# Performance work log

Hardware: AMD Instinct MI355X
Metric: run time of the kernel (lower is better)

The kernel has to match this reference:

```python
import jax, jax.numpy as jnp
import numpy as np
import math

B, C, N, T = 8, 128, 256, 64  # batch, d_model, nodes, timesteps
H = 8                          # attention heads
NUM_STEPS = 50                 # diffusion steps


def _conv2d(x, w, b):
    # Conv2d with kernel (1,3), padding (0,1); x: (B,C,N,T), w: (O,I,1,3)
    y = jax.lax.conv_general_dilated(x, w, (1, 1), [(0, 0), (1, 1)],
                                     dimension_numbers=('NCHW', 'OIHW', 'NCHW'))
    return y + b[None, :, None, None]


def _linear(x, w, b=None):
    y = jnp.einsum('...i,oi->...o', x, w)
    return y if b is None else y + b


def _ln(x, g, b, eps=1e-5):
    m = jnp.mean(x, -1, keepdims=True)
    v = jnp.var(x, -1, keepdims=True)
    return (x - m) * jax.lax.rsqrt(v + eps) * g + b


def _forward(step, x, adj, wq, bq, wk, bk, w1, b1, w2, b2, theta,
             ln0_g, ln0_b, ln1_g, ln1_b, p1_w, p1_b, p2_w, p2_b,
             dxc_w, dxc_b, dec_w, dec_b, dc1_w, dc1_b, dp2_w, dp2_b):
    dk = C // H
    sq = 1.0 / math.sqrt(dk)
    sc = 1.0 / math.sqrt(C)
    # ---- normalized graph Laplacian: D^{-1/2} A D^{-1/2} (get_laplacian, normalize=True)
    d = jnp.sum(adj, -1) ** -0.5
    Lap = adj * d[:, None] * d[None, :]  # (N,N)
    # ---- temporal attention with conv-derived Q/K (MultiHeadAttentionAwareTemporal)
    q = _conv2d(x, wq, bq).reshape(B, H, dk, N, T).transpose(0, 3, 1, 4, 2)  # (B,N,H,T,dk)
    k = _conv2d(x, wk, bk).reshape(B, H, dk, N, T).transpose(0, 3, 1, 4, 2)
    v = _linear(x.transpose(0, 2, 3, 1), w1, b1).reshape(B, N, T, H, dk).transpose(0, 1, 3, 2, 4)
    p = jax.nn.softmax(jnp.einsum('bnhtd,bnhsd->bnhts', q, k) * sq, axis=-1)
    o = jnp.einsum('bnhts,bnhsd->bnhtd', p, v).transpose(0, 1, 3, 2, 4).reshape(B, N, T, C)
    xp = x.transpose(0, 2, 3, 1) + _ln(_linear(o, w2, b2), ln0_g, ln0_b)  # (B,N,T,C)
    # ---- spatial attention GCN (Spatial_Attention_layer + spatialAttentionGCN)
    xt = xp.transpose(0, 2, 1, 3)  # (B,T,N,C)
    sat = jax.nn.softmax(jnp.einsum('btnf,btmf->btnm', xt, xt) * sc, axis=-1) * sc
    y = jnp.einsum('btnm,btmf->btnf', Lap[None, None] * sat, xt)
    y = jax.nn.relu(_linear(y, theta)).transpose(0, 2, 1, 3)  # (B,N,T,C)
    h = xp + _ln(y, ln1_g, ln1_b)
    # ---- diffusion step embedding (DiffusionEmbedding)
    dim = C // 2
    freqs = 10.0 ** (jnp.arange(dim, dtype=jnp.float32) / (dim - 1) * 4.0)
    tab = jnp.arange(NUM_STEPS, dtype=jnp.float32)[:, None] * freqs[None, :]
    tab = jnp.concatenate([jnp.sin(tab), jnp.cos(tab)], -1)  # (NUM_STEPS, C)
    e = jax.nn.silu(_linear(tab[step], p1_w, p1_b))
    e = jax.nn.silu(_linear(e, p2_w, p2_b))  # (B,C)
    h = h + e[:, None, None, :]
    # ---- Decoder: conv + sigmoid-gated add + relu + 1x1 projection to 2 channels
    enc = h.transpose(0, 3, 1, 2)  # (B,C,N,T)
    xh = _conv2d(enc, dxc_w, dxc_b)
    ec = _conv2d(enc, dec_w, dec_b)
    out = jax.nn.relu(xh + jax.nn.sigmoid(ec) + _conv2d(ec, dc1_w, dc1_b))
    out = jnp.einsum('bcnt,oc->bont', out, dp2_w) + dp2_b[None, :, None, None]  # (B,2,N,T)
    return out


def setup_inputs() -> dict:
    key = jax.random.key(0)
    ks = iter(jax.random.split(key, 40))
    s = 1.0 / math.sqrt(C)
    sk = 1.0 / math.sqrt(3 * C)

    def nrm(shape, scale):
        return jax.random.normal(next(ks), shape, jnp.float32) * scale

    return {
        'x': nrm((B, C, N, T), 1.0),
        'adj': jax.random.uniform(next(ks), (N, N), jnp.float32, 0.1, 1.0),
        'step': jax.random.randint(next(ks), (B,), 0, NUM_STEPS, jnp.int32),
        'wq': nrm((C, C, 1, 3), sk), 'bq': jnp.zeros((C,), jnp.float32),
        'wk': nrm((C, C, 1, 3), sk), 'bk': jnp.zeros((C,), jnp.float32),
        'w1': nrm((C, C), s), 'b1': jnp.zeros((C,), jnp.float32),
        'w2': nrm((C, C), s), 'b2': jnp.zeros((C,), jnp.float32),
        'theta': nrm((C, C), s),
        'ln0_g': jnp.ones((C,), jnp.float32), 'ln0_b': jnp.zeros((C,), jnp.float32),
        'ln1_g': jnp.ones((C,), jnp.float32), 'ln1_b': jnp.zeros((C,), jnp.float32),
        'p1_w': nrm((C, C), s), 'p1_b': jnp.zeros((C,), jnp.float32),
        'p2_w': nrm((C, C), s), 'p2_b': jnp.zeros((C,), jnp.float32),
        'dxc_w': nrm((C, C, 1, 3), sk), 'dxc_b': jnp.zeros((C,), jnp.float32),
        'dec_w': nrm((C, C, 1, 3), sk), 'dec_b': jnp.zeros((C,), jnp.float32),
        'dc1_w': nrm((C, C, 1, 3), sk), 'dc1_b': jnp.zeros((C,), jnp.float32),
        'dp2_w': nrm((2, C), s), 'dp2_b': jnp.zeros((2,), jnp.float32),
    }


def reference(x, adj, step, wq, bq, wk, bk, w1, b1, w2, b2, theta,
              ln0_g, ln0_b, ln1_g, ln1_b, p1_w, p1_b, p2_w, p2_b,
              dxc_w, dxc_b, dec_w, dec_b, dc1_w, dc1_b, dp2_w, dp2_b):
    return _forward(step, x, adj, wq, bq, wk, bk, w1, b1, w2, b2, theta,
                    ln0_g, ln0_b, ln1_g, ln1_b, p1_w, p1_b, p2_w, p2_b,
                    dxc_w, dxc_b, dec_w, dec_b, dc1_w, dc1_b, dp2_w, dp2_b)
```

## Files before the change

### kernel.cpp

```cpp
#include <hip/hip_runtime.h>
#include <hip/hip_bf16.h>

namespace {

constexpr int C = 128, N = 256, T = 64, Bsz = 8;
constexpr int TILE = T * C;
constexpr size_t BIGE = (size_t)Bsz * N * T * C;

typedef short v8s __attribute__((ext_vector_type(8)));
typedef float v4f __attribute__((ext_vector_type(4)));

__device__ __forceinline__ float bfu(unsigned short u) {
  unsigned int x = ((unsigned int)u) << 16;
  return __uint_as_float(x);
}
__device__ __forceinline__ unsigned short f2b(float v) {
  __hip_bfloat16 h = __float2bfloat16(v);
  return *(unsigned short*)&h;
}
__device__ __forceinline__ unsigned int pk2(float a, float b) {
  return (unsigned int)f2b(a) | ((unsigned int)f2b(b) << 16);
}
__device__ __forceinline__ float ld(const void* p, size_t i, int f32) {
  if (f32) return ((const float*)p)[i];
  return bfu(((const unsigned short*)p)[i]);
}
__device__ __forceinline__ float sigm(float x) { return 1.f / (1.f + __expf(-x)); }

__global__ __launch_bounds__(64) void k_sniff(const unsigned short* x, int* flag) {
  __shared__ int cnt[64];
  int tid = threadIdx.x;
  int c = 0;
  for (int u = 0; u < 8; ++u) {
    unsigned short v = x[tid * 8 + u];
    int e = (v >> 7) & 255;
    c += (e >= 97 && e <= 157) ? 1 : 0;
  }
  cnt[tid] = c;
  __syncthreads();
  if (tid == 0) {
    int s = 0;
    for (int i = 0; i < 64; ++i) s += cnt[i];
    flag[0] = (s < 435) ? 1 : 0;
  }
}

struct PrepArgs {
  const int* flag;
  const void *wq, *wk, *w1, *w2, *th, *dxc, *dec, *dc1;
  const void *bq, *bk, *b1, *b2, *l0g, *l0b, *l1g, *l1b, *dxcb, *decb, *dc1b, *dp2w, *dp2b;
  unsigned short *wqkB, *w1B, *w2B;
  __hip_bfloat16* thB;
  unsigned short *decWb, *dxcWb, *dc1Wb;
  float *bqk, *b1f, *b2f, *l0gf, *l0bf, *l1gf, *l1bf, *dxcbf, *decbf, *dc1bf, *dp2wf, *dp2bf;
};

__global__ __launch_bounds__(256) void k_prepall(
    PrepArgs a, const void* adj, float* lap, const int* step,
    const void* p1w, const void* p1b, const void* p2w, const void* p2b, float* e) {
  __shared__ float sh[256];
  __shared__ float e1[128];
  int f = a.flag[0];
  int blk = blockIdx.x, tid = threadIdx.x;
  if (blk < 128) {
    int idx = blk * 256 + tid;
    const int stride = 32768;
    for (int i = idx; i < 256 * 384; i += stride) {
      int o = i / 384, k = i - o * 384;
      int j = k >> 7, ii = k & 127;
      float v = (o < 128) ? ld(a.wq, (o * 128 + ii) * 3 + j, f)
                          : ld(a.wk, ((o - 128) * 128 + ii) * 3 + j, f);
      a.wqkB[i] = f2b(v);
    }
    for (int i = idx; i < 16384; i += stride) {
      a.w1B[i] = f2b(ld(a.w1, i, f));
      a.w2B[i] = f2b(ld(a.w2, i, f));
      a.thB[i] = __float2bfloat16(ld(a.th, i, f));
    }
    for (int i = idx; i < 16384; i += stride) {
      int o = i >> 7, ii = i & 127;
      int sbase = (o * 128 + ii) * 3;
#pragma unroll
      for (int j = 0; j < 3; ++j) {
        int dsti = o * 384 + j * 128 + ii;
        a.decWb[dsti] = f2b(ld(a.dec, sbase + j, f));
        a.dxcWb[dsti] = f2b(ld(a.dxc, sbase + j, f));
        a.dc1Wb[dsti] = f2b(ld(a.dc1, sbase + j, f));
      }
    }
    for (int i = idx; i < 256; i += stride) {
      a.bqk[i] = (i < 128) ? ld(a.bq, i, f) : ld(a.bk, i - 128, f);
      a.dp2wf[i] = ld(a.dp2w, i, f);
    }
    for (int i = idx; i < 128; i += stride) {
      a.b1f[i] = ld(a.b1, i, f);   a.b2f[i] = ld(a.b2, i, f);
      a.l0gf[i] = ld(a.l0g, i, f); a.l0bf[i] = ld(a.l0b, i, f);
      a.l1gf[i] = ld(a.l1g, i, f); a.l1bf[i] = ld(a.l1b, i, f);
      a.dxcbf[i] = ld(a.dxcb, i, f); a.decbf[i] = ld(a.decb, i, f); a.dc1bf[i] = ld(a.dc1b, i, f);
    }
    if (idx < 2) a.dp2bf[idx] = ld(a.dp2b, idx, f);
  } else if (blk < 192) {
    float s = 0.f;
    for (int m = 0; m < 256; ++m) s += ld(adj, tid * 256 + m, f);
    sh[tid] = 1.f / sqrtf(s);
    __syncthreads();
    int n0 = (blk - 128) * 4;
    for (int idx = tid; idx < 1024; idx += 256) {
      int n = n0 + (idx >> 8), m = idx & 255;
      lap[n * 256 + m] = ld(adj, n * 256 + m, f) * sh[n] * sh[m];
    }
  } else {
    int b = blk - 192;
    if (tid < 128) {
      float sv = (float)step[b];
      int i0 = tid & 63;
      float fr = powf(10.f, (float)i0 / 63.f * 4.f);
      float ang = sv * fr;
      sh[tid] = (tid < 64) ? sinf(ang) : cosf(ang);
    }
    __syncthreads();
    if (tid < 128) {
      float aa = ld(p1b, tid, f);
      for (int i = 0; i < 128; ++i) aa += sh[i] * ld(p1w, tid * 128 + i, f);
      aa = aa * sigm(aa);
      e1[tid] = aa;
    }
    __syncthreads();
    if (tid < 128) {
      float a2 = ld(p2b, tid, f);
      for (int i = 0; i < 128; ++i) a2 += e1[i] * ld(p2w, tid * 128 + i, f);
      e[b * 128 + tid] = a2 * sigm(a2);
    }
  }
}

constexpr int XBS = 136;
constexpr int VTS = 72;

__global__ __launch_bounds__(512, 4) void k_mega1(
    const void* xin, const int* flag,
    const unsigned short* wqkB, const float* bqk,
    const unsigned short* w1B, const float* b1f,
    const unsigned short* w2B, const float* b2f,
    const float* l0g, const float* l0b, float* g0) {
  int bn = blockIdx.x, b = bn >> 8, n = bn & 255;
  __shared__ unsigned short Xb[66 * XBS];
  __shared__ unsigned short qo[64 * XBS];
  __shared__ unsigned short kls[64 * XBS];
  __shared__ unsigned short vT[128 * VTS];
  __shared__ float pS[8 * 64], pQ[8 * 64];
  __shared__ float mrow[64], vrow[64];
  int tid = threadIdx.x;
  int wv = tid >> 6, lane = tid & 63, quad = lane >> 4, lr = lane & 15;
  int f = flag[0];
  int hb = wv * 16;
  const v8s zz = {0, 0, 0, 0, 0, 0, 0, 0};
  {
    size_t xoff = (size_t)b * C * N * T + (size_t)n * T;
    for (int idx = tid * 4; idx < TILE; idx += 2048) {
      int i = idx >> 6, t = idx & 63;
      unsigned short pk[4];
      if (f) {
        float4 v4 = *(const float4*)&((const float*)xin)[xoff + (size_t)i * N * T + t];
        pk[0] = f2b(v4.x); pk[1] = f2b(v4.y); pk[2] = f2b(v4.z); pk[3] = f2b(v4.w);
      } else {
        ushort4 u4 = *(const ushort4*)&((const unsigned short*)xin)[xoff + (size_t)i * N * T + t];
        pk[0] = u4.x; pk[1] = u4.y; pk[2] = u4.z; pk[3] = u4.w;
      }
#pragma unroll
      for (int u = 0; u < 4; ++u) Xb[(t + u + 1) * XBS + i] = pk[u];
    }
    if (tid < 128) { Xb[tid] = 0; Xb[65 * XBS + tid] = 0; }
  }
  __syncthreads();
  {
    int mt0 = wv * 2;
    v4f acc[2][4];
#pragma unroll
    for (int mi = 0; mi < 2; ++mi)
#pragma unroll
      for (int nt = 0; nt < 4; ++nt) acc[mi][nt] = (v4f){0.f, 0.f, 0.f, 0.f};
    for (int j = 0; j < 3; ++j) {
#pragma unroll
      for (int kt = 0; kt < 4; ++kt) {
        int ko = j * 128 + kt * 32 + quad * 8;
        v8s a0 = *(const v8s*)&wqkB[(mt0 * 16 + lr) * 384 + ko];
        v8s a1 = *(const v8s*)&wqkB[((mt0 + 1) * 16 + lr) * 384 + ko];
        int bko = kt * 32 + quad * 8;
#pragma unroll
        for (int nt = 0; nt < 4; ++nt) {
          v8s bb = *(const v8s*)&Xb[(nt * 16 + lr + j) * XBS + bko];
          acc[0][nt] = __builtin_amdgcn_mfma_f32_16x16x32_bf16(a0, bb, acc[0][nt], 0, 0, 0);
          acc[1][nt] = __builtin_amdgcn_mfma_f32_16x16x32_bf16(a1, bb, acc[1][nt], 0, 0, 0);
        }
      }
    }
    unsigned short* dst = (wv < 4) ? qo : kls;
#pragma unroll
    for (int mi = 0; mi < 2; ++mi) {
      int og = (mt0 + mi) * 16 + quad * 4;
      int oo = og & 127;
#pragma unroll
      for (int nt = 0; nt < 4; ++nt) {
        int t = nt * 16 + lr;
        *(unsigned int*)&dst[t * XBS + oo] =
            pk2(acc[mi][nt][0] + bqk[og], acc[mi][nt][1] + bqk[og + 1]);
        *(unsigned int*)&dst[t * XBS + oo + 2] =
            pk2(acc[mi][nt][2] + bqk[og + 2], acc[mi][nt][3] + bqk[og + 3]);
      }
    }
  }
  {
    v4f av[4];
#pragma unroll
    for (int nt = 0; nt < 4; ++nt) av[nt] = (v4f){0.f, 0.f, 0.f, 0.f};
#pragma unroll
    for (int kt = 0; kt < 4; ++kt) {
      int ko = kt * 32 + quad * 8;
      v8s a = *(const v8s*)&w1B[(wv * 16 + lr) * 128 + ko];
#pragma unroll
      for (int nt = 0; nt < 4; ++nt) {
        v8s bb = *(const v8s*)&Xb[(nt * 16 + lr + 1) * XBS + ko];
        av[nt] = __builtin_amdgcn_mfma_f32_16x16x32_bf16(a, bb, av[nt], 0, 0, 0);
      }
    }
#pragma unroll
    for (int nt = 0; nt < 4; ++nt) {
      int t = nt * 16 + lr;
#pragma unroll
      for (int r = 0; r < 4; ++r) {
        int o = hb + quad * 4 + r;
        vT[o * VTS + t] = f2b(av[nt][r] + b1f[o]);
      }
    }
  }
  __syncthreads();
  {
    v4f sa[4][4];
#pragma unroll
    for (int ms = 0; ms < 4; ++ms)
#pragma unroll
      for (int nt = 0; nt < 4; ++nt) sa[ms][nt] = (v4f){0.f, 0.f, 0.f, 0.f};
    {
      v8s afs[4], bfs[4];
#pragma unroll
      for (int ms = 0; ms < 4; ++ms)
        afs[ms] = (quad < 2) ? *(const v8s*)&kls[(ms * 16 + lr) * XBS + hb + quad * 8] : zz;
#pragma unroll
      for (int nt = 0; nt < 4; ++nt)
        bfs[nt] = (quad < 2) ? *(const v8s*)&qo[(nt * 16 + lr) * XBS + hb + quad * 8] : zz;
#pragma unroll
      for (int ms = 0; ms < 4; ++ms)
#pragma unroll
        for (int nt = 0; nt < 4; ++nt)
          sa[ms][nt] = __builtin_amdgcn_mfma_f32_16x16x32_bf16(afs[ms], bfs[nt], sa[ms][nt], 0, 0, 0);
    }
#pragma unroll
    for (int nt = 0; nt < 4; ++nt) {
      float mx = -1e30f;
#pragma unroll
      for (int ms = 0; ms < 4; ++ms)
#pragma unroll
        for (int r = 0; r < 4; ++r) {
          float v = sa[ms][nt][r] * 0.25f;
          sa[ms][nt][r] = v;
          mx = fmaxf(mx, v);
        }
      mx = fmaxf(mx, __shfl_xor(mx, 16, 64));
      mx = fmaxf(mx, __shfl_xor(mx, 32, 64));
      float ssum = 0.f;
#pragma unroll
      for (int ms = 0; ms < 4; ++ms)
#pragma unroll
        for (int r = 0; r < 4; ++r) {
          float e = __expf(sa[ms][nt][r] - mx);
          sa[ms][nt][r] = e;
          ssum += e;
        }
      ssum += __shfl_xor(ssum, 16, 64);
      ssum += __shfl_xor(ssum, 32, 64);
      float inv = 1.f / ssum;
#pragma unroll
      for (int ms = 0; ms < 4; ++ms)
#pragma unroll
        for (int r = 0; r < 4; ++r) sa[ms][nt][r] *= inv;
    }
    v4f ov[4];
#pragma unroll
    for (int nt = 0; nt < 4; ++nt) ov[nt] = (v4f){0.f, 0.f, 0.f, 0.f};
#pragma unroll
    for (int kt = 0; kt < 2; ++kt) {
      unsigned int pA[4][2], pB[4][2];
#pragma unroll
      for (int nt = 0; nt < 4; ++nt) {
#pragma unroll
        for (int h = 0; h < 2; ++h) {
          pA[nt][h] = pk2(sa[2 * kt][nt][2 * h], sa[2 * kt][nt][2 * h + 1]);
          pB[nt][h] = pk2(sa[2 * kt + 1][nt][2 * h], sa[2 * kt + 1][nt][2 * h + 1]);
        }
      }
      v8s aV = *(const v8s*)&vT[(hb + lr) * VTS + kt * 32 + quad * 8];
#pragma unroll
      for (int nt = 0; nt < 4; ++nt) {
        union { unsigned int u[4]; v8s s; } bu;
#pragma unroll
        for (int w = 0; w < 4; ++w) {
          int src = (2 * (quad & 1) + (w >> 1)) * 16 + lr;
          unsigned int x0 = (unsigned int)__shfl((int)pA[nt][w & 1], src, 64);
          unsigned int x1 = (unsigned int)__shfl((int)pB[nt][w & 1], src, 64);
          bu.u[w] = (quad >> 1) ? x1 : x0;
        }
        ov[nt] = __builtin_amdgcn_mfma_f32_16x16x32_bf16(aV, bu.s, ov[nt], 0, 0, 0);
      }
    }
#pragma unroll
    for (int nt = 0; nt < 4; ++nt) {
      int t = nt * 16 + lr;
      *(unsigned int*)&qo[t * XBS + hb + quad * 4] = pk2(ov[nt][0], ov[nt][1]);
      *(unsigned int*)&qo[t * XBS + hb + quad * 4 + 2] = pk2(ov[nt][2], ov[nt][3]);
    }
  }
  __syncthreads();
  v4f aw[4];
  {
#pragma unroll
    for (int nt = 0; nt < 4; ++nt) aw[nt] = (v4f){0.f, 0.f, 0.f, 0.f};
#pragma unroll
    for (int kt = 0; kt < 4; ++kt) {
      int ko = kt * 32 + quad * 8;
      v8s a = *(const v8s*)&w2B[(wv * 16 + lr) * 128 + ko];
#pragma unroll
      for (int nt = 0; nt < 4; ++nt) {
        v8s bb = *(const v8s*)&qo[(nt * 16 + lr) * XBS + ko];
        aw[nt] = __builtin_amdgcn_mfma_f32_16x16x32_bf16(a, bb, aw[nt], 0, 0, 0);
      }
    }
    int ob = hb + quad * 4;
#pragma unroll
    for (int nt = 0; nt < 4; ++nt) {
      float s = 0.f, q2 = 0.f;
#pragma unroll
      for (int r = 0; r < 4; ++r) {
        aw[nt][r] += b2f[ob + r];
        s += aw[nt][r];
        q2 += aw[nt][r] * aw[nt][r];
      }
      s += __shfl_xor(s, 16, 64);  s += __shfl_xor(s, 32, 64);
      q2 += __shfl_xor(q2, 16, 64); q2 += __shfl_xor(q2, 32, 64);
      if (quad == 0) {
        pS[wv * 64 + nt * 16 + lr] = s;
        pQ[wv * 64 + nt * 16 + lr] = q2;
      }
    }
  }
  __syncthreads();
  if (tid < 64) {
    float s = 0.f, q2 = 0.f;
#pragma unroll
    for (int w = 0; w < 8; ++w) { s += pS[w * 64 + tid]; q2 += pQ[w * 64 + tid]; }
    float mm = s * (1.f / 128.f);
    mrow[tid] = mm;
    vrow[tid] = rsqrtf(q2 * (1.f / 128.f) - mm * mm + 1e-5f);
  }
  __syncthreads();
  {
    int ob = hb + quad * 4;
    float gg[4], bb2[4];
#pragma unroll
    for (int r = 0; r < 4; ++r) { gg[r] = l0g[ob + r]; bb2[r] = l0b[ob + r]; }
    float* dst = g0 + (size_t)bn * TILE;
#pragma unroll
    for (int nt = 0; nt < 4; ++nt) {
      int t = nt * 16 + lr;
      float m = mrow[t], rs = vrow[t];
      ushort4 xr = *(const ushort4*)&Xb[(t + 1) * XBS + ob];
      float4 o4;
      o4.x = (aw[nt][0] - m) * rs * gg[0] + bb2[0] + bfu(xr.x);
      o4.y = (aw[nt][1] - m) * rs * gg[1] + bb2[1] + bfu(xr.y);
      o4.z = (aw[nt][2] - m) * rs * gg[2] + bb2[2] + bfu(xr.z);
      o4.w = (aw[nt][3] - m) * rs * gg[3] + bb2[3] + bfu(xr.w);
      *(float4*)&dst[t * 128 + ob] = o4;
    }
  }
}

constexpr int XS = 136;
constexpr int TS = 264;

__global__ __launch_bounds__(512, 1) void k_megasp(
    const float* g0, const float* lap, const unsigned short* thB,
    const float* l1g, const float* l1b, const float* e, unsigned short* g0b) {
  int bt = blockIdx.x, b = bt >> 6, t = bt & 63;
  __shared__ unsigned short R1[256 * XS];
  __shared__ unsigned short R2[256 * XS];
  __shared__ float pS[8][256], pQ[8][256];
  __shared__ float mrow[256], vrow[256];
  unsigned short* Xhi = R1;
  unsigned short* Xlo = R2;
  unsigned short* Xt = R2;
  unsigned short* Pld = R1;
  int tid = threadIdx.x;
  int wv = tid >> 6, lane = tid & 63, quad = lane >> 4, lr = lane & 15;
  int wrow0 = wv * 32;
  const float sc = 0.08838834764831845f;
  {
    size_t base = (size_t)b * (N * (size_t)TILE) + (size_t)t * 128;
    for (int idx = tid * 4; idx < 32768; idx += 2048) {
      int n = idx >> 7, c = idx & 127;
      float4 v4 = *(const float4*)&g0[base + (size_t)n * TILE + c];
      ushort4 h, l;
      h.x = f2b(v4.x); l.x = f2b(v4.x - bfu(h.x));
      h.y = f2b(v4.y); l.y = f2b(v4.y - bfu(h.y));
      h.z = f2b(v4.z); l.z = f2b(v4.z - bfu(h.z));
      h.w = f2b(v4.w); l.w = f2b(v4.w - bfu(h.w));
      *(ushort4*)&Xhi[n * XS + c] = h;
      *(ushort4*)&Xlo[n * XS + c] = l;
    }
  }
  __syncthreads();
  v4f acc[2][16];
#pragma unroll
  for (int mi = 0; mi < 2; ++mi)
#pragma unroll
    for (int nt = 0; nt < 16; ++nt) acc[mi][nt] = (v4f){0.f, 0.f, 0.f, 0.f};
  for (int kt = 0; kt < 4; ++kt) {
    int ko = kt * 32 + quad * 8;
    v8s ah0 = *(const v8s*)&Xhi[(wrow0 + lr) * XS + ko];
    v8s al0 = *(const v8s*)&Xlo[(wrow0 + lr) * XS + ko];
    v8s ah1 = *(const v8s*)&Xhi[(wrow0 + 16 + lr) * XS + ko];
    v8s al1 = *(const v8s*)&Xlo[(wrow0 + 16 + lr) * XS + ko];
#pragma unroll
    for (int nt = 0; nt < 16; ++nt) {
      v8s bh = *(const v8s*)&Xhi[(nt * 16 + lr) * XS + ko];
      v8s bl = *(const v8s*)&Xlo[(nt * 16 + lr) * XS + ko];
      acc[0][nt] = __builtin_amdgcn_mfma_f32_16x16x32_bf16(ah0, bh, acc[0][nt], 0, 0, 0);
      acc[0][nt] = __builtin_amdgcn_mfma_f32_16x16x32_bf16(ah0, bl, acc[0][nt], 0, 0, 0);
      acc[0][nt] = __builtin_amdgcn_mfma_f32_16x16x32_bf16(al0, bh, acc[0][nt], 0, 0, 0);
      acc[1][nt] = __builtin_amdgcn_mfma_f32_16x16x32_bf16(ah1, bh, acc[1][nt], 0, 0, 0);
      acc[1][nt] = __builtin_amdgcn_mfma_f32_16x16x32_bf16(ah1, bl, acc[1][nt], 0, 0, 0);
      acc[1][nt] = __builtin_amdgcn_mfma_f32_16x16x32_bf16(al1, bh, acc[1][nt], 0, 0, 0);
    }
  }
  __syncthreads();
  for (int task = tid; task < 8192; task += 512) {
    int c = task & 127, n0 = (task >> 7) * 4;
    ushort4 w;
    w.x = Xhi[(n0 + 0) * XS + c];
    w.y = Xhi[(n0 + 1) * XS + c];
    w.z = Xhi[(n0 + 2) * XS + c];
    w.w = Xhi[(n0 + 3) * XS + c];
    *(ushort4*)&Xt[c * TS + n0] = w;
  }
  __syncthreads();
  unsigned int pk1[2][8][2];
#pragma unroll
  for (int mi = 0; mi < 2; ++mi) {
#pragma unroll
    for (int r = 0; r < 4; ++r) {
      int row = wrow0 + 16 * mi + quad * 4 + r;
      float mx = -1e30f;
#pragma unroll
      for (int nt = 0; nt < 16; ++nt) {
        acc[mi][nt][r] *= sc;
        mx = fmaxf(mx, acc[mi][nt][r]);
      }
#pragma unroll
      for (int m = 8; m > 0; m >>= 1) mx = fmaxf(mx, __shfl_xor(mx, m, 16));
      float ex[16];
      float ssum = 0.f;
#pragma unroll
      for (int nt = 0; nt < 16; ++nt) { ex[nt] = __expf(acc[mi][nt][r] - mx); ssum += ex[nt]; }
#pragma unroll
      for (int m = 8; m > 0; m >>= 1) ssum += __shfl_xor(ssum, m, 16);
      float inv = sc / ssum;
      const float* lrow = lap + row * 256 + lr;
#pragma unroll
      for (int nt = 0; nt < 8; ++nt)
        Pld[row * XS + nt * 16 + lr] = f2b(ex[nt] * inv * lrow[nt * 16]);
#pragma unroll
      for (int nt = 8; nt < 16; ++nt) {
        unsigned int hbw = (unsigned int)f2b(ex[nt] * inv * lrow[nt * 16]);
        if ((r & 1) == 0) pk1[mi][nt - 8][r >> 1] = hbw;
        else pk1[mi][nt - 8][r >> 1] |= hbw << 16;
      }
    }
  }
  v4f acc2[2][8];
#pragma unroll
  for (int mi = 0; mi < 2; ++mi)
#pragma unroll
    for (int nt = 0; nt < 8; ++nt) acc2[mi][nt] = (v4f){0.f, 0.f, 0.f, 0.f};
#pragma unroll
  for (int h = 0; h < 2; ++h) {
    if (h == 1) {
#pragma unroll
      for (int mi = 0; mi < 2; ++mi) {
        int rowb = wrow0 + 16 * mi + quad * 4;
#pragma unroll
        for (int k = 0; k < 8; ++k) {
          int col = k * 16 + lr;
          unsigned int u0 = pk1[mi][k][0], u1 = pk1[mi][k][1];
          Pld[(rowb + 0) * XS + col] = (unsigned short)u0;
          Pld[(rowb + 1) * XS + col] = (unsigned short)(u0 >> 16);
          Pld[(rowb + 2) * XS + col] = (unsigned short)u1;
          Pld[(rowb + 3) * XS + col] = (unsigned short)(u1 >> 16);
        }
      }
    }
    for (int kt = 0; kt < 4; ++kt) {
      int ko = kt * 32 + quad * 8;
      v8s pa0 = *(const v8s*)&Pld[(wrow0 + lr) * XS + ko];
      v8s pa1 = *(const v8s*)&Pld[(wrow0 + 16 + lr) * XS + ko];
#pragma unroll
      for (int nt = 0; nt < 8; ++nt) {
        v8s xb = *(const v8s*)&Xt[(nt * 16 + lr) * TS + h * 128 + ko];
        acc2[0][nt] = __builtin_amdgcn_mfma_f32_16x16x32_bf16(pa0, xb, acc2[0][nt], 0, 0, 0);
        acc2[1][nt] = __builtin_amdgcn_mfma_f32_16x16x32_bf16(pa1, xb, acc2[1][nt], 0, 0, 0);
      }
    }
  }
  __syncthreads();
  unsigned short* yB = R2;
  unsigned short* ths = R1;
#pragma unroll
  for (int mi = 0; mi < 2; ++mi) {
    int nb = wrow0 + 16 * mi + quad * 4;
#pragma unroll
    for (int nt = 0; nt < 8; ++nt) {
      int c = nt * 16 + lr;
#pragma unroll
      for (int r = 0; r < 4; ++r)
        yB[(nb + r) * XS + c] = f2b(acc2[mi][nt][r]);
    }
  }
  for (int idx = tid * 8; idx < 16384; idx += 4096) {
    int o = idx >> 7, k = idx & 127;
    *(uint4*)&ths[o * 136 + k] = *(const uint4*)&thB[idx];
  }
  __syncthreads();
  v4f acc3[16];
#pragma unroll
  for (int nt = 0; nt < 16; ++nt) acc3[nt] = (v4f){0.f, 0.f, 0.f, 0.f};
#pragma unroll
  for (int kt = 0; kt < 4; ++kt) {
    int ko = kt * 32 + quad * 8;
    v8s a = *(const v8s*)&ths[(wv * 16 + lr) * 136 + ko];
#pragma unroll
    for (int nt = 0; nt < 16; ++nt) {
      v8s bb = *(const v8s*)&yB[(nt * 16 + lr) * XS + ko];
      acc3[nt] = __builtin_amdgcn_mfma_f32_16x16x32_bf16(a, bb, acc3[nt], 0, 0, 0);
    }
  }
#pragma unroll
  for (int nt = 0; nt < 16; ++nt) {
    float s = 0.f, q2 = 0.f;
#pragma unroll
    for (int r = 0; r < 4; ++r) {
      float v = fmaxf(acc3[nt][r], 0.f);
      acc3[nt][r] = v;
      s += v; q2 += v * v;
    }
    s += __shfl_xor(s, 16, 64);  s += __shfl_xor(s, 32, 64);
    q2 += __shfl_xor(q2, 16, 64); q2 += __shfl_xor(q2, 32, 64);
    if (quad == 0) { pS[wv][nt * 16 + lr] = s; pQ[wv][nt * 16 + lr] = q2; }
  }
  __syncthreads();
  if (tid < 256) {
    float s = 0.f, q2 = 0.f;
#pragma unroll
    for (int w = 0; w < 8; ++w) { s += pS[w][tid]; q2 += pQ[w][tid]; }
    float mm = s * (1.f / 128.f);
    mrow[tid] = mm;
    vrow[tid] = rsqrtf(q2 * (1.f / 128.f) - mm * mm + 1e-5f);
  }
  __syncthreads();
  {
    int o0 = wv * 16 + quad * 4;
    float gg[4], bb2[4], ev[4];
    const float* eb = e + b * 128;
#pragma unroll
    for (int r = 0; r < 4; ++r) { gg[r] = l1g[o0 + r]; bb2[r] = l1b[o0 + r]; ev[r] = eb[o0 + r]; }
#pragma unroll
    for (int nt = 0; nt < 16; ++nt) {
      int n = nt * 16 + lr;
      float m = mrow[n], rs = vrow[n];
      size_t ga = ((size_t)(b * 256 + n)) * TILE + (size_t)t * 128 + o0;
      float4 xa = *(const float4*)&g0[ga];
      ushort4 pk;
      pk.x = f2b((acc3[nt][0] - m) * rs * gg[0] + bb2[0] + xa.x + ev[0]);
      pk.y = f2b((acc3[nt][1] - m) * rs * gg[1] + bb2[1] + xa.y + ev[1]);
      pk.z = f2b((acc3[nt][2] - m) * rs * gg[2] + bb2[2] + xa.z + ev[2]);
      pk.w = f2b((acc3[nt][3] - m) * rs * gg[3] + bb2[3] + xa.w + ev[3]);
      *(ushort4*)&g0b[ga] = pk;
    }
  }
}

__global__ __launch_bounds__(512, 4) void k_megadec(
    const unsigned short* g0b, const unsigned short* decW, const float* decb,
    const unsigned short* dxcW, const float* dxcb,
    const unsigned short* dc1W, const float* dc1b,
    const float* dp2w, const float* dp2b, const int* flag, void* outv) {
  int bn = blockIdx.x, b = bn >> 8, n = bn & 255;
  int f32o = flag[0];
  __shared__ unsigned short Xm[66 * XBS];
  __shared__ unsigned short E2[66 * XBS];
  __shared__ float pb0[8][64], pb1[8][64];
  int tid = threadIdx.x;
  int wv = tid >> 6, lane = tid & 63, quad = lane >> 4, lr = lane & 15;
  int m0 = wv * 16;
  const unsigned short* gp = g0b + (size_t)bn * TILE;
  for (int idx = tid * 8; idx < TILE; idx += 4096) {
    int t = idx >> 7, c = idx & 127;
    *(uint4*)&Xm[(t + 1) * XBS + c] = *(const uint4*)&gp[idx];
  }
  if (tid < 128) {
    Xm[tid] = 0; Xm[65 * XBS + tid] = 0;
    E2[tid] = 0; E2[65 * XBS + tid] = 0;
  }
  __syncthreads();
  v4f acc[4];
  float ecv[4][4];
#pragma unroll
  for (int nt = 0; nt < 4; ++nt) acc[nt] = (v4f){0.f, 0.f, 0.f, 0.f};
  for (int j = 0; j < 3; ++j) {
#pragma unroll
    for (int kt = 0; kt < 4; ++kt) {
      v8s a = *(const v8s*)&decW[(m0 + lr) * 384 + j * 128 + kt * 32 + quad * 8];
      int bko = kt * 32 + quad * 8;
#pragma unroll
      for (int nt = 0; nt < 4; ++nt) {
        v8s bb = *(const v8s*)&Xm[(nt * 16 + lr + j) * XBS + bko];
        acc[nt] = __builtin_amdgcn_mfma_f32_16x16x32_bf16(a, bb, acc[nt], 0, 0, 0);
      }
    }
  }
#pragma unroll
  for (int nt = 0; nt < 4; ++nt) {
    int t = nt * 16 + lr;
    int o = m0 + quad * 4;
    ushort4 pk;
#pragma unroll
    for (int r = 0; r < 4; ++r) {
      float v = acc[nt][r] + decb[o + r];
      ecv[nt][r] = v;
      ((unsigned short*)&pk)[r] = f2b(v);
    }
    *(ushort4*)&E2[(t + 1) * XBS + o] = pk;
  }
  __syncthreads();
  v4f ax[4], ac[4];
#pragma unroll
  for (int nt = 0; nt < 4; ++nt) { ax[nt] = (v4f){0.f,0.f,0.f,0.f}; ac[nt] = (v4f){0.f,0.f,0.f,0.f}; }
  for (int j = 0; j < 3; ++j) {
#pragma unroll
    for (int kt = 0; kt < 4; ++kt) {
      int wo = (m0 + lr) * 384 + j * 128 + kt * 32 + quad * 8;
      v8s a1 = *(const v8s*)&dxcW[wo];
      v8s a2 = *(const v8s*)&dc1W[wo];
      int bko = kt * 32 + quad * 8;
#pragma unroll
      for (int nt = 0; nt < 4; ++nt) {
        int row = (nt * 16 + lr + j) * XBS + bko;
        v8s b1 = *(const v8s*)&Xm[row];
        v8s b2v = *(const v8s*)&E2[row];
        ax[nt] = __builtin_amdgcn_mfma_f32_16x16x32_bf16(a1, b1, ax[nt], 0, 0, 0);
        ac[nt] = __builtin_amdgcn_mfma_f32_16x16x32_bf16(a2, b2v, ac[nt], 0, 0, 0);
      }
    }
  }
#pragma unroll
  for (int nt = 0; nt < 4; ++nt) {
    float p0 = 0.f, p1 = 0.f;
#pragma unroll
    for (int r = 0; r < 4; ++r) {
      int o = m0 + quad * 4 + r;
      float v = fmaxf(ax[nt][r] + dxcb[o] + sigm(ecv[nt][r]) + ac[nt][r] + dc1b[o], 0.f);
      p0 += v * dp2w[o];
      p1 += v * dp2w[128 + o];
    }
    p0 += __shfl_xor(p0, 16, 64); p0 += __shfl_xor(p0, 32, 64);
    p1 += __shfl_xor(p1, 16, 64); p1 += __shfl_xor(p1, 32, 64);
    if (quad == 0) { pb0[wv][nt * 16 + lr] = p0; pb1[wv][nt * 16 + lr] = p1; }
  }
  __syncthreads();
  if (tid < 128) {
    int ch = tid >> 6, t = tid & 63;
    float s = 0.f;
    if (ch == 0) { for (int w = 0; w < 8; ++w) s += pb0[w][t]; s += dp2b[0]; }
    else         { for (int w = 0; w < 8; ++w) s += pb1[w][t]; s += dp2b[1]; }
    size_t oi = ((size_t)(b * 2 + ch) * 256 + n) * 64 + t;
    if (f32o) ((float*)outv)[oi] = s;
    else ((__hip_bfloat16*)outv)[oi] = __float2bfloat16(s);
  }
}

}

extern "C" void kernel_launch(void* const* d_in, const int* in_sizes, int n_in,
                              void* d_out, int out_size, void* d_ws, size_t ws_size,
                              hipStream_t stream) {
  (void)in_sizes; (void)n_in; (void)out_size; (void)ws_size;
  const void* x    = d_in[0];
  const void* adj  = d_in[1];
  const int*  step = (const int*)d_in[2];
  const void* wq   = d_in[3];
  const void* bq   = d_in[4];
  const void* wk   = d_in[5];
  const void* bk   = d_in[6];
  const void* w1   = d_in[7];
  const void* b1   = d_in[8];
  const void* w2   = d_in[9];
  const void* b2   = d_in[10];
  const void* th   = d_in[11];
  const void* l0g  = d_in[12];
  const void* l0b  = d_in[13];
  const void* l1g  = d_in[14];
  const void* l1b  = d_in[15];
  const void* p1w  = d_in[16];
  const void* p1b  = d_in[17];
  const void* p2w  = d_in[18];
  const void* p2b  = d_in[19];
  const void* dxcw = d_in[20];
  const void* dxcb = d_in[21];
  const void* decw = d_in[22];
  const void* decb = d_in[23];
  const void* dc1w = d_in[24];
  const void* dc1b = d_in[25];
  const void* dp2w = d_in[26];
  const void* dp2b = d_in[27];

  float* ws = (float*)d_ws;
  int* flag = (int*)ws;
  float* p = ws + 16;
  float* e     = p; p += 1024;
  float* lap   = p; p += 65536;
  float* wqkBv = p; p += 49152;
  float* w1Bv  = p; p += 8192;
  float* w2Bv  = p; p += 8192;
  float* thBv  = p; p += 8192;
  float* decWv = p; p += 24576;
  float* dxcWv = p; p += 24576;
  float* dc1Wv = p; p += 24576;
  float* bqk   = p; p += 256;
  float* b1f   = p; p += 128;
  float* b2f   = p; p += 128;
  float* l0gf  = p; p += 128;
  float* l0bf  = p; p += 128;
  float* l1gf  = p; p += 128;
  float* l1bf  = p; p += 128;
  float* dxcbf = p; p += 128;
  float* decbf = p; p += 128;
  float* dc1bf = p; p += 128;
  float* dp2wf = p; p += 256;
  float* dp2bf = p; p += 8;
  size_t off = (size_t)(p - ws);
  off = (off + 127) & ~(size_t)127;
  float* xf = ws + off;
  float* g0 = xf + BIGE;
  unsigned short* g0b = (unsigned short*)xf;

  PrepArgs pa;
  pa.flag = flag;
  pa.wq = wq; pa.wk = wk; pa.w1 = w1; pa.w2 = w2; pa.th = th;
  pa.dxc = dxcw; pa.dec = decw; pa.dc1 = dc1w;
  pa.bq = bq; pa.bk = bk; pa.b1 = b1; pa.b2 = b2;
  pa.l0g = l0g; pa.l0b = l0b; pa.l1g = l1g; pa.l1b = l1b;
  pa.dxcb = dxcb; pa.decb = decb; pa.dc1b = dc1b; pa.dp2w = dp2w; pa.dp2b = dp2b;
  pa.wqkB = (unsigned short*)wqkBv;
  pa.w1B = (unsigned short*)w1Bv;
  pa.w2B = (unsigned short*)w2Bv;
  pa.thB = (__hip_bfloat16*)thBv;
  pa.decWb = (unsigned short*)decWv;
  pa.dxcWb = (unsigned short*)dxcWv;
  pa.dc1Wb = (unsigned short*)dc1Wv;
  pa.bqk = bqk; pa.b1f = b1f; pa.b2f = b2f;
  pa.l0gf = l0gf; pa.l0bf = l0bf; pa.l1gf = l1gf; pa.l1bf = l1bf;
  pa.dxcbf = dxcbf; pa.decbf = decbf; pa.dc1bf = dc1bf; pa.dp2wf = dp2wf; pa.dp2bf = dp2bf;

  k_sniff<<<1, 64, 0, stream>>>((const unsigned short*)x, flag);
  k_prepall<<<200, 256, 0, stream>>>(pa, adj, lap, step, p1w, p1b, p2w, p2b, e);

  k_mega1<<<2048, 512, 0, stream>>>(x, flag, (const unsigned short*)wqkBv, bqk,
                                    (const unsigned short*)w1Bv, b1f,
                                    (const unsigned short*)w2Bv, b2f, l0gf, l0bf, g0);
  k_megasp<<<512, 512, 0, stream>>>(g0, lap, (const unsigned short*)thBv,
                                    l1gf, l1bf, e, g0b);
  k_megadec<<<2048, 512, 0, stream>>>(g0b, (const unsigned short*)decWv, decbf,
                                      (const unsigned short*)dxcWv, dxcbf,
                                      (const unsigned short*)dc1Wv, dc1bf,
                                      dp2wf, dp2bf, flag, d_out);
}
```

Before: 411.1 us.

## Split g0 into bf16 hi/lo planes and run spatial kernel with 1024 threads

```diff
diff --git a/kernel.cpp b/kernel.cpp
--- a/kernel.cpp
+++ b/kernel.cpp
@@ -142,7 +142,8 @@
     const unsigned short* wqkB, const float* bqk,
     const unsigned short* w1B, const float* b1f,
     const unsigned short* w2B, const float* b2f,
-    const float* l0g, const float* l0b, float* g0) {
+    const float* l0g, const float* l0b,
+    unsigned short* g0h, unsigned short* g0l) {
   int bn = blockIdx.x, b = bn >> 8, n = bn & 255;
   __shared__ unsigned short Xb[66 * XBS];
   __shared__ unsigned short qo[64 * XBS];
@@ -368,18 +369,27 @@
     float gg[4], bb2[4];
 #pragma unroll
     for (int r = 0; r < 4; ++r) { gg[r] = l0g[ob + r]; bb2[r] = l0b[ob + r]; }
-    float* dst = g0 + (size_t)bn * TILE;
+    unsigned short* dh = g0h + (size_t)bn * TILE;
+    unsigned short* dl = g0l + (size_t)bn * TILE;
 #pragma unroll
     for (int nt = 0; nt < 4; ++nt) {
       int t = nt * 16 + lr;
       float m = mrow[t], rs = vrow[t];
       ushort4 xr = *(const ushort4*)&Xb[(t + 1) * XBS + ob];
-      float4 o4;
-      o4.x = (aw[nt][0] - m) * rs * gg[0] + bb2[0] + bfu(xr.x);
-      o4.y = (aw[nt][1] - m) * rs * gg[1] + bb2[1] + bfu(xr.y);
-      o4.z = (aw[nt][2] - m) * rs * gg[2] + bb2[2] + bfu(xr.z);
-      o4.w = (aw[nt][3] - m) * rs * gg[3] + bb2[3] + bfu(xr.w);
-      *(float4*)&dst[t * 128 + ob] = o4;
+      float o4[4];
+      o4[0] = (aw[nt][0] - m) * rs * gg[0] + bb2[0] + bfu(xr.x);
+      o4[1] = (aw[nt][1] - m) * rs * gg[1] + bb2[1] + bfu(xr.y);
+      o4[2] = (aw[nt][2] - m) * rs * gg[2] + bb2[2] + bfu(xr.z);
+      o4[3] = (aw[nt][3] - m) * rs * gg[3] + bb2[3] + bfu(xr.w);
+      ushort4 hh, ll;
+#pragma unroll
+      for (int r = 0; r < 4; ++r) {
+        unsigned short h = f2b(o4[r]);
+        ((unsigned short*)&hh)[r] = h;
+        ((unsigned short*)&ll)[r] = f2b(o4[r] - bfu(h));
+      }
+      *(ushort4*)&dh[t * 128 + ob] = hh;
+      *(ushort4*)&dl[t * 128 + ob] = ll;
     }
   }
 }
@@ -387,8 +397,9 @@
 constexpr int XS = 136;
 constexpr int TS = 264;
 
-__global__ __launch_bounds__(512, 1) void k_megasp(
-    const float* g0, const float* lap, const unsigned short* thB,
+__global__ __launch_bounds__(1024, 4) void k_megasp(
+    const unsigned short* g0h, const unsigned short* g0l,
+    const float* lap, const unsigned short* thB,
     const float* l1g, const float* l1b, const float* e, unsigned short* g0b) {
   int bt = blockIdx.x, b = bt >> 6, t = bt & 63;
   __shared__ unsigned short R1[256 * XS];
@@ -401,48 +412,36 @@
   unsigned short* Pld = R1;
   int tid = threadIdx.x;
   int wv = tid >> 6, lane = tid & 63, quad = lane >> 4, lr = lane & 15;
-  int wrow0 = wv * 32;
+  int wrow0 = wv * 16;
   const float sc = 0.08838834764831845f;
   {
     size_t base = (size_t)b * (N * (size_t)TILE) + (size_t)t * 128;
-    for (int idx = tid * 4; idx < 32768; idx += 2048) {
+    for (int idx = tid * 4; idx < 32768; idx += 4096) {
       int n = idx >> 7, c = idx & 127;
-      float4 v4 = *(const float4*)&g0[base + (size_t)n * TILE + c];
-      ushort4 h, l;
-      h.x = f2b(v4.x); l.x = f2b(v4.x - bfu(h.x));
-      h.y = f2b(v4.y); l.y = f2b(v4.y - bfu(h.y));
-      h.z = f2b(v4.z); l.z = f2b(v4.z - bfu(h.z));
-      h.w = f2b(v4.w); l.w = f2b(v4.w - bfu(h.w));
-      *(ushort4*)&Xhi[n * XS + c] = h;
-      *(ushort4*)&Xlo[n * XS + c] = l;
-    }
-  }
-  __syncthreads();
-  v4f acc[2][16];
-#pragma unroll
-  for (int mi = 0; mi < 2; ++mi)
-#pragma unroll
-    for (int nt = 0; nt < 16; ++nt) acc[mi][nt] = (v4f){0.f, 0.f, 0.f, 0.f};
+      size_t ga = base + (size_t)n * TILE + c;
+      *(ushort4*)&Xhi[n * XS + c] = *(const ushort4*)&g0h[ga];
+      *(ushort4*)&Xlo[n * XS + c] = *(const ushort4*)&g0l[ga];
+    }
+  }
+  __syncthreads();
+  v4f acc[16];
+#pragma unroll
+  for (int nt = 0; nt < 16; ++nt) acc[nt] = (v4f){0.f, 0.f, 0.f, 0.f};
   for (int kt = 0; kt < 4; ++kt) {
     int ko = kt * 32 + quad * 8;
     v8s ah0 = *(const v8s*)&Xhi[(wrow0 + lr) * XS + ko];
     v8s al0 = *(const v8s*)&Xlo[(wrow0 + lr) * XS + ko];
-    v8s ah1 = *(const v8s*)&Xhi[(wrow0 + 16 + lr) * XS + ko];
-    v8s al1 = *(const v8s*)&Xlo[(wrow0 + 16 + lr) * XS + ko];
 #pragma unroll
     for (int nt = 0; nt < 16; ++nt) {
       v8s bh = *(const v8s*)&Xhi[(nt * 16 + lr) * XS + ko];
       v8s bl = *(const v8s*)&Xlo[(nt * 16 + lr) * XS + ko];
-      acc[0][nt] = __builtin_amdgcn_mfma_f32_16x16x32_bf16(ah0, bh, acc[0][nt], 0, 0, 0);
-      acc[0][nt] = __builtin_amdgcn_mfma_f32_16x16x32_bf16(ah0, bl, acc[0][nt], 0, 0, 0);
-      acc[0][nt] = __builtin_amdgcn_mfma_f32_16x16x32_bf16(al0, bh, acc[0][nt], 0, 0, 0);
-      acc[1][nt] = __builtin_amdgcn_mfma_f32_16x16x32_bf16(ah1, bh, acc[1][nt], 0, 0, 0);
-      acc[1][nt] = __builtin_amdgcn_mfma_f32_16x16x32_bf16(ah1, bl, acc[1][nt], 0, 0, 0);
-      acc[1][nt] = __builtin_amdgcn_mfma_f32_16x16x32_bf16(al1, bh, acc[1][nt], 0, 0, 0);
-    }
-  }
-  __syncthreads();
-  for (int task = tid; task < 8192; task += 512) {
+      acc[nt] = __builtin_amdgcn_mfma_f32_16x16x32_bf16(ah0, bh, acc[nt], 0, 0, 0);
+      acc[nt] = __builtin_amdgcn_mfma_f32_16x16x32_bf16(ah0, bl, acc[nt], 0, 0, 0);
+      acc[nt] = __builtin_amdgcn_mfma_f32_16x16x32_bf16(al0, bh, acc[nt], 0, 0, 0);
+    }
+  }
+  __syncthreads();
+  for (int task = tid; task < 8192; task += 1024) {
     int c = task & 127, n0 = (task >> 7) * 4;
     ushort4 w;
     w.x = Xhi[(n0 + 0) * XS + c];
@@ -452,107 +451,98 @@
     *(ushort4*)&Xt[c * TS + n0] = w;
   }
   __syncthreads();
-  unsigned int pk1[2][8][2];
-#pragma unroll
-  for (int mi = 0; mi < 2; ++mi) {
-#pragma unroll
-    for (int r = 0; r < 4; ++r) {
-      int row = wrow0 + 16 * mi + quad * 4 + r;
-      float mx = -1e30f;
-#pragma unroll
-      for (int nt = 0; nt < 16; ++nt) {
-        acc[mi][nt][r] *= sc;
-        mx = fmaxf(mx, acc[mi][nt][r]);
-      }
-#pragma unroll
-      for (int m = 8; m > 0; m >>= 1) mx = fmaxf(mx, __shfl_xor(mx, m, 16));
-      float ex[16];
-      float ssum = 0.f;
-#pragma unroll
-      for (int nt = 0; nt < 16; ++nt) { ex[nt] = __expf(acc[mi][nt][r] - mx); ssum += ex[nt]; }
-#pragma unroll
-      for (int m = 8; m > 0; m >>= 1) ssum += __shfl_xor(ssum, m, 16);
-      float inv = sc / ssum;
-      const float* lrow = lap + row * 256 + lr;
-#pragma unroll
-      for (int nt = 0; nt < 8; ++nt)
-        Pld[row * XS + nt * 16 + lr] = f2b(ex[nt] * inv * lrow[nt * 16]);
-#pragma unroll
-      for (int nt = 8; nt < 16; ++nt) {
-        unsigned int hbw = (unsigned int)f2b(ex[nt] * inv * lrow[nt * 16]);
-        if ((r & 1) == 0) pk1[mi][nt - 8][r >> 1] = hbw;
-        else pk1[mi][nt - 8][r >> 1] |= hbw << 16;
-      }
-    }
-  }
-  v4f acc2[2][8];
-#pragma unroll
-  for (int mi = 0; mi < 2; ++mi)
-#pragma unroll
-    for (int nt = 0; nt < 8; ++nt) acc2[mi][nt] = (v4f){0.f, 0.f, 0.f, 0.f};
+  unsigned int pk1[8][2];
+#pragma unroll
+  for (int r = 0; r < 4; ++r) {
+    int row = wrow0 + quad * 4 + r;
+    float mx = -1e30f;
+#pragma unroll
+    for (int nt = 0; nt < 16; ++nt) {
+      acc[nt][r] *= sc;
+      mx = fmaxf(mx, acc[nt][r]);
+    }
+#pragma unroll
+    for (int m = 8; m > 0; m >>= 1) mx = fmaxf(mx, __shfl_xor(mx, m, 16));
+    float ex[16];
+    float ssum = 0.f;
+#pragma unroll
+    for (int nt = 0; nt < 16; ++nt) { ex[nt] = __expf(acc[nt][r] - mx); ssum += ex[nt]; }
+#pragma unroll
+    for (int m = 8; m > 0; m >>= 1) ssum += __shfl_xor(ssum, m, 16);
+    float inv = sc / ssum;
+    const float* lrow = lap + row * 256 + lr;
+#pragma unroll
+    for (int nt = 0; nt < 8; ++nt)
+      Pld[row * XS + nt * 16 + lr] = f2b(ex[nt] * inv * lrow[nt * 16]);
+#pragma unroll
+    for (int nt = 8; nt < 16; ++nt) {
+      unsigned int hbw = (unsigned int)f2b(ex[nt] * inv * lrow[nt * 16]);
+      if ((r & 1) == 0) pk1[nt - 8][r >> 1] = hbw;
+      else pk1[nt - 8][r >> 1] |= hbw << 16;
+    }
+  }
+  v4f acc2[8];
+#pragma unroll
+  for (int nt = 0; nt < 8; ++nt) acc2[nt] = (v4f){0.f, 0.f, 0.f, 0.f};
 #pragma unroll
   for (int h = 0; h < 2; ++h) {
     if (h == 1) {
-#pragma unroll
-      for (int mi = 0; mi < 2; ++mi) {
-        int rowb = wrow0 + 16 * mi + quad * 4;
-#pragma unroll
-        for (int k = 0; k < 8; ++k) {
-          int col = k * 16 + lr;
-          unsigned int u0 = pk1[mi][k][0], u1 = pk1[mi][k][1];
-          Pld[(rowb + 0) * XS + col] = (unsigned short)u0;
-          Pld[(rowb + 1) * XS + col] = (unsigned short)(u0 >> 16);
-          Pld[(rowb + 2) * XS + col] = (unsigned short)u1;
-          Pld[(rowb + 3) * XS + col] = (unsigned short)(u1 >> 16);
-        }
+      int rowb = wrow0 + quad * 4;
+#pragma unroll
+      for (int k = 0; k < 8; ++k) {
+        int col = k * 16 + lr;
+        unsigned int u0 = pk1[k][0], u1 = pk1[k][1];
+        Pld[(rowb + 0) * XS + col] = (unsigned short)u0;
+        Pld[(rowb + 1) * XS + col] = (unsigned short)(u0 >> 16);
+        Pld[(rowb + 2) * XS + col] = (unsigned short)u1;
+        Pld[(rowb + 3) * XS + col] = (unsigned short)(u1 >> 16);
       }
     }
     for (int kt = 0; kt < 4; ++kt) {
       int ko = kt * 32 + quad * 8;
       v8s pa0 = *(const v8s*)&Pld[(wrow0 + lr) * XS + ko];
-      v8s pa1 = *(const v8s*)&Pld[(wrow0 + 16 + lr) * XS + ko];
 #pragma unroll
       for (int nt = 0; nt < 8; ++nt) {
         v8s xb = *(const v8s*)&Xt[(nt * 16 + lr) * TS + h * 128 + ko];
-        acc2[0][nt] = __builtin_amdgcn_mfma_f32_16x16x32_bf16(pa0, xb, acc2[0][nt], 0, 0, 0);
-        acc2[1][nt] = __builtin_amdgcn_mfma_f32_16x16x32_bf16(pa1, xb, acc2[1][nt], 0, 0, 0);
+        acc2[nt] = __builtin_amdgcn_mfma_f32_16x16x32_bf16(pa0, xb, acc2[nt], 0, 0, 0);
       }
     }
   }
   __syncthreads();
   unsigned short* yB = R2;
   unsigned short* ths = R1;
-#pragma unroll
-  for (int mi = 0; mi < 2; ++mi) {
-    int nb = wrow0 + 16 * mi + quad * 4;
+  {
+    int nb = wrow0 + quad * 4;
 #pragma unroll
     for (int nt = 0; nt < 8; ++nt) {
       int c = nt * 16 + lr;
 #pragma unroll
       for (int r = 0; r < 4; ++r)
-        yB[(nb + r) * XS + c] = f2b(acc2[mi][nt][r]);
-    }
-  }
-  for (int idx = tid * 8; idx < 16384; idx += 4096) {
+        yB[(nb + r) * XS + c] = f2b(acc2[nt][r]);
+    }
+  }
+  for (int idx = tid * 8; idx < 16384; idx += 8192) {
     int o = idx >> 7, k = idx & 127;
     *(uint4*)&ths[o * 136 + k] = *(const uint4*)&thB[idx];
   }
   __syncthreads();
-  v4f acc3[16];
-#pragma unroll
-  for (int nt = 0; nt < 16; ++nt) acc3[nt] = (v4f){0.f, 0.f, 0.f, 0.f};
+  int ot = wv & 7, nh = wv >> 3;
+  v4f acc3[8];
+#pragma unroll
+  for (int nt = 0; nt < 8; ++nt) acc3[nt] = (v4f){0.f, 0.f, 0.f, 0.f};
 #pragma unroll
   for (int kt = 0; kt < 4; ++kt) {
     int ko = kt * 32 + quad * 8;
-    v8s a = *(const v8s*)&ths[(wv * 16 + lr) * 136 + ko];
-#pragma unroll
-    for (int nt = 0; nt < 16; ++nt) {
-      v8s bb = *(const v8s*)&yB[(nt * 16 + lr) * XS + ko];
+    v8s a = *(const v8s*)&ths[(ot * 16 + lr) * 136 + ko];
+#pragma unroll
+    for (int nt = 0; nt < 8; ++nt) {
+      int ng = nh * 8 + nt;
+      v8s bb = *(const v8s*)&yB[(ng * 16 + lr) * XS + ko];
       acc3[nt] = __builtin_amdgcn_mfma_f32_16x16x32_bf16(a, bb, acc3[nt], 0, 0, 0);
     }
   }
 #pragma unroll
-  for (int nt = 0; nt < 16; ++nt) {
+  for (int nt = 0; nt < 8; ++nt) {
     float s = 0.f, q2 = 0.f;
 #pragma unroll
     for (int r = 0; r < 4; ++r) {
@@ -562,7 +552,10 @@
     }
     s += __shfl_xor(s, 16, 64);  s += __shfl_xor(s, 32, 64);
     q2 += __shfl_xor(q2, 16, 64); q2 += __shfl_xor(q2, 32, 64);
-    if (quad == 0) { pS[wv][nt * 16 + lr] = s; pQ[wv][nt * 16 + lr] = q2; }
+    if (quad == 0) {
+      int n = (nh * 8 + nt) * 16 + lr;
+      pS[ot][n] = s; pQ[ot][n] = q2;
+    }
   }
   __syncthreads();
   if (tid < 256) {
@@ -575,22 +568,23 @@
   }
   __syncthreads();
   {
-    int o0 = wv * 16 + quad * 4;
+    int o0 = ot * 16 + quad * 4;
     float gg[4], bb2[4], ev[4];
     const float* eb = e + b * 128;
 #pragma unroll
     for (int r = 0; r < 4; ++r) { gg[r] = l1g[o0 + r]; bb2[r] = l1b[o0 + r]; ev[r] = eb[o0 + r]; }
 #pragma unroll
-    for (int nt = 0; nt < 16; ++nt) {
-      int n = nt * 16 + lr;
+    for (int nt = 0; nt < 8; ++nt) {
+      int n = (nh * 8 + nt) * 16 + lr;
       float m = mrow[n], rs = vrow[n];
       size_t ga = ((size_t)(b * 256 + n)) * TILE + (size_t)t * 128 + o0;
-      float4 xa = *(const float4*)&g0[ga];
+      ushort4 xh = *(const ushort4*)&g0h[ga];
+      ushort4 xl = *(const ushort4*)&g0l[ga];
       ushort4 pk;
-      pk.x = f2b((acc3[nt][0] - m) * rs * gg[0] + bb2[0] + xa.x + ev[0]);
-      pk.y = f2b((acc3[nt][1] - m) * rs * gg[1] + bb2[1] + xa.y + ev[1]);
-      pk.z = f2b((acc3[nt][2] - m) * rs * gg[2] + bb2[2] + xa.z + ev[2]);
-      pk.w = f2b((acc3[nt][3] - m) * rs * gg[3] + bb2[3] + xa.w + ev[3]);
+      pk.x = f2b((acc3[nt][0] - m) * rs * gg[0] + bb2[0] + bfu(xh.x) + bfu(xl.x) + ev[0]);
+      pk.y = f2b((acc3[nt][1] - m) * rs * gg[1] + bb2[1] + bfu(xh.y) + bfu(xl.y) + ev[1]);
+      pk.z = f2b((acc3[nt][2] - m) * rs * gg[2] + bb2[2] + bfu(xh.z) + bfu(xl.z) + ev[2]);
+      pk.w = f2b((acc3[nt][3] - m) * rs * gg[3] + bb2[3] + bfu(xh.w) + bfu(xl.w) + ev[3]);
       *(ushort4*)&g0b[ga] = pk;
     }
   }
@@ -757,8 +751,9 @@
   size_t off = (size_t)(p - ws);
   off = (off + 127) & ~(size_t)127;
   float* xf = ws + off;
-  float* g0 = xf + BIGE;
   unsigned short* g0b = (unsigned short*)xf;
+  unsigned short* g0h = (unsigned short*)(xf + BIGE);
+  unsigned short* g0l = g0h + BIGE;
 
   PrepArgs pa;
   pa.flag = flag;
@@ -783,9 +778,10 @@
 
   k_mega1<<<2048, 512, 0, stream>>>(x, flag, (const unsigned short*)wqkBv, bqk,
                                     (const unsigned short*)w1Bv, b1f,
-                                    (const unsigned short*)w2Bv, b2f, l0gf, l0bf, g0);
-  k_megasp<<<512, 512, 0, stream>>>(g0, lap, (const unsigned short*)thBv,
-                                    l1gf, l1bf, e, g0b);
+                                    (const unsigned short*)w2Bv, b2f, l0gf, l0bf,
+                                    g0h, g0l);
+  k_megasp<<<512, 1024, 0, stream>>>(g0h, g0l, lap, (const unsigned short*)thBv,
+                                     l1gf, l1bf, e, g0b);
   k_megadec<<<2048, 512, 0, stream>>>(g0b, (const unsigned short*)decWv, decbf,
                                       (const unsigned short*)dxcWv, dxcbf,
                                       (const unsigned short*)dc1Wv, dc1bf,
```

After: 425.0 us. 1.03x slower.
